# Optimization experiments

Hardware: AMD Instinct MI355X
Metric: run time of the kernel (lower is better)

## Reference

```python
import jax, jax.numpy as jnp
import numpy as np

N, E, F_IN, H, G, K = 50000, 800000, 64, 200, 256, 3


def setup_inputs() -> dict:
    key = jax.random.key(0)
    ks = jax.random.split(key, 12)
    x = jax.random.normal(ks[0], (N, F_IN), jnp.float32)
    edge_index = jax.random.randint(ks[1], (2, E), 0, N, dtype=jnp.int64)
    batch = jnp.sort(jax.random.randint(ks[2], (N,), 0, G, dtype=jnp.int64))
    lmax = 1.5 + jax.random.uniform(ks[3], (G,), jnp.float32)  # per-graph lambda_max

    def lin(k, i, o):
        return (jax.random.normal(k, (K, i, o), jnp.float32) / np.sqrt(i)).astype(jnp.float32)

    return dict(
        x=x, edge_index=edge_index, batch=batch, lmax=lmax,
        W1=lin(ks[4], F_IN, H), b1=jnp.zeros((H,), jnp.float32),
        W2=lin(ks[5], H, H),    b2=jnp.zeros((H,), jnp.float32),
        W3=lin(ks[6], H, H),    b3=jnp.zeros((H,), jnp.float32),
        W4=lin(ks[7], H, H),    b4=jnp.zeros((H,), jnp.float32),
        fc_w=(jax.random.normal(ks[8], (2 * H, 2), jnp.float32) / np.sqrt(2 * H)).astype(jnp.float32),
        fc_b=jnp.zeros((2,), jnp.float32),
    )


def reference(x, edge_index, batch, lmax, W1, b1, W2, b2, W3, b3, W4, b4, fc_w, fc_b):
    n = x.shape[0]
    g = lmax.shape[0]
    src, dst = edge_index[0], edge_index[1]

    # PyG ChebConv sym normalization: L_hat = 2/lambda_max * (I - D^-1/2 A D^-1/2) - I
    deg = jax.ops.segment_sum(jnp.ones(src.shape[0], x.dtype), src, num_segments=n)
    dis = jnp.where(deg > 0, jnp.maximum(deg, 1.0) ** -0.5, 0.0)  # deg^{-1/2}, inf -> 0
    scale = 2.0 / lmax                                            # [G]
    w = -dis[src] * dis[dst] * scale[batch[src]]                  # off-diagonal edge weights [E]
    diag = scale[batch] - 1.0                                     # diagonal of L_hat, [N]

    def prop(h):  # L_hat @ h via sparse scatter
        return jax.ops.segment_sum(w[:, None] * h[src], dst, num_segments=n) + diag[:, None] * h

    def cheb(h, W, b):  # K=3 Chebyshev recurrence
        Tx0 = h
        Tx1 = prop(h)
        Tx2 = 2.0 * prop(Tx1) - Tx0
        return Tx0 @ W[0] + Tx1 @ W[1] + Tx2 @ W[2] + b

    h = jax.nn.relu(cheb(x, W1, b1))
    h = jax.nn.relu(cheb(h, W2, b2))
    h = jax.nn.relu(cheb(h, W3, b3))
    h = jax.nn.relu(cheb(h, W4, b4))

    cnt = jax.ops.segment_sum(jnp.ones(n, h.dtype), batch, num_segments=g)
    pooled_mean = jax.ops.segment_sum(h, batch, num_segments=g) / jnp.maximum(cnt, 1.0)[:, None]
    pooled_max = jax.ops.segment_max(h, batch, num_segments=g)
    z = jnp.concatenate([pooled_mean, pooled_max], axis=1) @ fc_w + fc_b
    return jax.nn.log_softmax(z, axis=1)
```

## Files before the change

kernel.cpp:

```cpp
#include <hip/hip_runtime.h>
#include <math.h>

#define NN 50000
#define MP 50048
#define NE 800000
#define FIN 64
#define HD 200
#define NG 256
#define SCAN_B 256
#define KPAD 224
#define NT 13
#define HB 12544
#define PER_B 3125

typedef _Float16 h16;
typedef __attribute__((ext_vector_type(8))) _Float16 half8;
typedef __attribute__((ext_vector_type(4))) float float4v;
typedef unsigned long long u64;

__global__ __launch_bounds__(256) void k_hist(const int* __restrict__ idx,
                                              unsigned* __restrict__ partial, int E) {
    __shared__ unsigned h[HB];
    int tid = threadIdx.x;
    int e0 = blockIdx.x * PER_B;
    int v[13];
#pragma unroll
    for (int j = 0; j < 13; ++j) {
        int o = j * 256 + tid;
        v[j] = (o < PER_B) ? idx[e0 + o] : -1;
    }
#pragma unroll
    for (int pass = 0; pass < 2; ++pass) {
        for (int t = tid; t < HB; t += 256) h[t] = 0;
        __syncthreads();
        int lo = pass * (2 * HB);
#pragma unroll
        for (int j = 0; j < 13; ++j) {
            int vv = v[j] - lo;
            if (vv >= 0 && vv < 2 * HB)
                atomicAdd(&h[vv >> 1], (vv & 1) ? 0x10000u : 1u);
        }
        __syncthreads();
        unsigned* pb = partial + ((size_t)pass * 256 + blockIdx.x) * HB;
        for (int t = tid; t < HB; t += 256) pb[t] = h[t];
        __syncthreads();
    }
}

__global__ void k_hreduce(const unsigned* __restrict__ partial, int* __restrict__ cnt, int n) {
    int i = blockIdx.x * blockDim.x + threadIdx.x;
    if (i >= 2 * HB) return;
    int pass = i / HB, p = i - pass * HB;
    const unsigned* pb = partial + (size_t)pass * 256 * HB + p;
    unsigned s = 0;
    for (int b = 0; b < 256; ++b) s += pb[(size_t)b * HB];
    int n0 = pass * 2 * HB + 2 * p;
    if (n0 < n)     cnt[n0]     = (int)(s & 0xffffu);
    if (n0 + 1 < n) cnt[n0 + 1] = (int)(s >> 16);
}

__global__ void k_hscan(unsigned* __restrict__ partial, int* __restrict__ cnt, int n) {
    int i = blockIdx.x * blockDim.x + threadIdx.x;
    if (i >= 2 * HB) return;
    int pass = i / HB, p = i - pass * HB;
    unsigned* pb = partial + (size_t)pass * 256 * HB + p;
    unsigned run = 0;
    for (int b = 0; b < 256; ++b) {
        unsigned c = pb[(size_t)b * HB];
        pb[(size_t)b * HB] = run;
        run += c;
    }
    int n0 = pass * 2 * HB + 2 * p;
    if (n0 < n)     cnt[n0]     = (int)(run & 0xffffu);
    if (n0 + 1 < n) cnt[n0 + 1] = (int)(run >> 16);
}

__global__ void k_node_prep(const int* __restrict__ degi, const int* __restrict__ batch,
                            const float* __restrict__ lmax, float* __restrict__ dis,
                            float* __restrict__ qs, float* __restrict__ diag, int n) {
    int i = blockIdx.x * blockDim.x + threadIdx.x;
    if (i < n) {
        int d = degi[i];
        float di = (d > 0) ? (1.0f / sqrtf((float)d)) : 0.0f;
        float sc = 2.0f / lmax[batch[i]];
        dis[i] = di;
        qs[i] = -di * sc;
        diag[i] = sc - 1.0f;
    }
}

__global__ void k_scan1(const int* __restrict__ cnt, int* __restrict__ excl,
                        int* __restrict__ bsum, int n) {
    __shared__ int sh[SCAN_B];
    int tid = threadIdx.x;
    int i = blockIdx.x * SCAN_B + tid;
    int v = (i < n) ? cnt[i] : 0;
    sh[tid] = v;
    __syncthreads();
    for (int off = 1; off < SCAN_B; off <<= 1) {
        int t = (tid >= off) ? sh[tid - off] : 0;
        __syncthreads();
        sh[tid] += t;
        __syncthreads();
    }
    if (i < n) excl[i] = sh[tid] - v;
    if (tid == SCAN_B - 1) bsum[blockIdx.x] = sh[tid];
}

__global__ void k_scan2(int* __restrict__ bsum, int nb) {
    __shared__ int sh[SCAN_B];
    int tid = threadIdx.x;
    int v = (tid < nb) ? bsum[tid] : 0;
    sh[tid] = v;
    __syncthreads();
    for (int off = 1; off < SCAN_B; off <<= 1) {
        int t = (tid >= off) ? sh[tid - off] : 0;
        __syncthreads();
        sh[tid] += t;
        __syncthreads();
    }
    if (tid < nb) bsum[tid] = sh[tid] - v;
}

__global__ void k_scan3(int* __restrict__ excl, const int* __restrict__ bsum, int n) {
    int i = blockIdx.x * SCAN_B + threadIdx.x;
    if (i < n) excl[i] += bsum[blockIdx.x];
}

__global__ __launch_bounds__(256) void k_fillcsr2(
    const int* __restrict__ src, const int* __restrict__ dst,
    const float* __restrict__ qs, const float* __restrict__ dis,
    const int* __restrict__ rowst, const unsigned* __restrict__ hpart,
    u64* __restrict__ csr, int E) {
    __shared__ unsigned lrank[HB];
    int tid = threadIdx.x;
    int e0 = blockIdx.x * PER_B;
    int vs[13], vd[13];
#pragma unroll
    for (int j = 0; j < 13; ++j) {
        int o = j * 256 + tid;
        vs[j] = (o < PER_B) ? src[e0 + o] : -1;
        vd[j] = (o < PER_B) ? dst[e0 + o] : -1;
    }
#pragma unroll
    for (int pass = 0; pass < 2; ++pass) {
        for (int t = tid; t < HB; t += 256) lrank[t] = 0;
        __syncthreads();
        int lo = pass * (2 * HB);
        const unsigned* base = hpart + ((size_t)pass * 256 + blockIdx.x) * HB;
#pragma unroll
        for (int j = 0; j < 13; ++j) {
            int vv = vd[j] - lo;
            if (vv >= 0 && vv < 2 * HB) {
                unsigned old = atomicAdd(&lrank[vv >> 1], (vv & 1) ? 0x10000u : 1u);
                unsigned rank = (vv & 1) ? (old >> 16) : (old & 0xffffu);
                unsigned bs = base[vv >> 1];
                unsigned b = (vv & 1) ? (bs >> 16) : (bs & 0xffffu);
                int s = vs[j], d = vd[j];
                int pos = rowst[d] + (int)b + (int)rank;
                float w = qs[s] * dis[d];
                csr[pos] = (unsigned)s | ((u64)__float_as_uint(w) << 32);
            }
        }
        __syncthreads();
    }
}

__global__ void k_split(const float* __restrict__ x, h16* __restrict__ x16, int total) {
    int i = blockIdx.x * blockDim.x + threadIdx.x;
    if (i < total) x16[i] = (h16)x[i];
}

__global__ void k_wprep(const float* __restrict__ W, h16* __restrict__ out,
                        int fin, int ksteps, int total) {
    int idx = blockIdx.x * blockDim.x + threadIdx.x;
    if (idx >= total) return;
    int kk = idx & 31;
    int r = idx >> 5;
    int nn = r % 208;
    int r2 = r / 208;
    int ks = r2 % ksteps;
    int seg = r2 / ksteps;
    int k = ks * 32 + kk;
    out[idx] = (nn < HD && k < fin) ? (h16)W[((size_t)seg * fin + k) * HD + nn] : (h16)0.f;
}

__global__ void k_bounds(const int* __restrict__ batch, int* __restrict__ gstart, int n) {
    int g = blockIdx.x * blockDim.x + threadIdx.x;
    if (g > NG) return;
    if (g == NG) { gstart[NG] = n; return; }
    int lo = 0, hi = n;
    while (lo < hi) {
        int mid = (lo + hi) >> 1;
        if (batch[mid] < g) lo = mid + 1; else hi = mid;
    }
    gstart[g] = lo;
}

__global__ __launch_bounds__(256) void k_gather(
    const int* __restrict__ rowstart, const int* __restrict__ rowcnt,
    const u64* __restrict__ csr, const float* __restrict__ diag,
    const h16* __restrict__ hin16, const h16* __restrict__ h016,
    h16* __restrict__ hout16, int s16, int lsh, int n, int mode) {
    int per = 256 >> lsh;
    int i = blockIdx.x * per + (threadIdx.x >> lsh);
    if (i >= n) return;
    int lane = threadIdx.x & ((1 << lsh) - 1);
    int c0 = lane * 4;
    if (c0 >= s16) return;
    int start = rowstart[i], cnt = rowcnt[i];
    float a0 = 0.f, a1 = 0.f, a2 = 0.f, a3 = 0.f;
    union U { uint2 u; h16 h[4]; };
    const u64* cp = csr + start;
    int k = 0;
    for (; k + 7 < cnt; k += 8) {
        u64 e[8];
#pragma unroll
        for (int j = 0; j < 8; ++j) e[j] = cp[k + j];
        U p[8];
#pragma unroll
        for (int j = 0; j < 8; ++j)
            p[j].u = *(const uint2*)(hin16 + (size_t)(unsigned)(e[j] & 0xffffffffu) * s16 + c0);
#pragma unroll
        for (int j = 0; j < 8; ++j) {
            float w = __uint_as_float((unsigned)(e[j] >> 32));
            a0 += w * (float)p[j].h[0];
            a1 += w * (float)p[j].h[1];
            a2 += w * (float)p[j].h[2];
            a3 += w * (float)p[j].h[3];
        }
    }
    for (; k + 1 < cnt; k += 2) {
        u64 e0 = cp[k], e1 = cp[k + 1];
        U p0, p1;
        p0.u = *(const uint2*)(hin16 + (size_t)(unsigned)(e0 & 0xffffffffu) * s16 + c0);
        p1.u = *(const uint2*)(hin16 + (size_t)(unsigned)(e1 & 0xffffffffu) * s16 + c0);
        float w0 = __uint_as_float((unsigned)(e0 >> 32));
        float w1 = __uint_as_float((unsigned)(e1 >> 32));
        a0 += w0 * (float)p0.h[0] + w1 * (float)p1.h[0];
        a1 += w0 * (float)p0.h[1] + w1 * (float)p1.h[1];
        a2 += w0 * (float)p0.h[2] + w1 * (float)p1.h[2];
        a3 += w0 * (float)p0.h[3] + w1 * (float)p1.h[3];
    }
    if (k < cnt) {
        u64 e0 = cp[k];
        U p0;
        p0.u = *(const uint2*)(hin16 + (size_t)(unsigned)(e0 & 0xffffffffu) * s16 + c0);
        float w0 = __uint_as_float((unsigned)(e0 >> 32));
        a0 += w0 * (float)p0.h[0];
        a1 += w0 * (float)p0.h[1];
        a2 += w0 * (float)p0.h[2];
        a3 += w0 * (float)p0.h[3];
    }
    float dg = diag[i];
    U hs; hs.u = *(const uint2*)(hin16 + (size_t)i * s16 + c0);
    float v0 = a0 + dg * (float)hs.h[0];
    float v1 = a1 + dg * (float)hs.h[1];
    float v2 = a2 + dg * (float)hs.h[2];
    float v3 = a3 + dg * (float)hs.h[3];
    if (mode == 1) {
        U h0; h0.u = *(const uint2*)(h016 + (size_t)i * s16 + c0);
        v0 = 2.f * v0 - (float)h0.h[0];
        v1 = 2.f * v1 - (float)h0.h[1];
        v2 = 2.f * v2 - (float)h0.h[2];
        v3 = 2.f * v3 - (float)h0.h[3];
    }
    U o;
    o.h[0] = (h16)v0; o.h[1] = (h16)v1; o.h[2] = (h16)v2; o.h[3] = (h16)v3;
    *(uint2*)(hout16 + (size_t)i * s16 + c0) = o.u;
}

__global__ __launch_bounds__(256) void k_gemm16(
    const h16* __restrict__ A0, const h16* __restrict__ A1, const h16* __restrict__ A2,
    int strideA, int ksteps,
    const h16* __restrict__ Wt, const float* __restrict__ bias,
    h16* __restrict__ out16, int n) {
    int tid = threadIdx.x;
    int wave = tid >> 6, lane = tid & 63;
    int nq = lane & 15, quad = lane >> 4;
    int row0 = (blockIdx.x * 4 + wave) * 32;
    const h16* Aseg[3] = {A0, A1, A2};

    float4v acc[2][NT];
#pragma unroll
    for (int r = 0; r < 2; r++)
#pragma unroll
        for (int t = 0; t < NT; t++) acc[r][t] = (float4v)0.f;

    for (int seg = 0; seg < 3; ++seg) {
        const h16* Ab = Aseg[seg] + (size_t)(row0 + nq) * strideA + quad * 8;
        const h16* Bb = Wt + (size_t)seg * ksteps * 208 * 32 + (size_t)nq * 32 + quad * 8;
        for (int ks = 0; ks < ksteps; ++ks) {
            half8 af0 = *(const half8*)(Ab + ks * 32);
            half8 af1 = *(const half8*)(Ab + 16 * strideA + ks * 32);
            const h16* Bk = Bb + (size_t)ks * 208 * 32;
#pragma unroll
            for (int t = 0; t < NT; ++t) {
                half8 bf = *(const half8*)(Bk + t * 16 * 32);
                acc[0][t] = __builtin_amdgcn_mfma_f32_16x16x32_f16(af0, bf, acc[0][t], 0, 0, 0);
                acc[1][t] = __builtin_amdgcn_mfma_f32_16x16x32_f16(af1, bf, acc[1][t], 0, 0, 0);
            }
        }
    }
#pragma unroll
    for (int r = 0; r < 2; ++r) {
        int rowb = row0 + r * 16 + quad * 4;
#pragma unroll
        for (int t = 0; t < NT; ++t) {
            int col = t * 16 + nq;
            if (col >= HD) continue;
            float bj = bias[col];
#pragma unroll
            for (int g = 0; g < 4; ++g) {
                int row = rowb + g;
                if (row < n)
                    out16[(size_t)row * KPAD + col] = (h16)fmaxf(acc[r][t][g] + bj, 0.0f);
            }
        }
    }
}

__global__ __launch_bounds__(256) void k_pool_fc(
    const h16* __restrict__ Hf, const int* __restrict__ gstart,
    const float* __restrict__ fcw, const float* __restrict__ fcb,
    float* __restrict__ out) {
    __shared__ float red[8];
    int g = blockIdx.x;
    int j = threadIdx.x;
    int i0 = gstart[g], i1 = gstart[g + 1];
    float s0 = 0.f, s1 = 0.f, s2 = 0.f, s3 = 0.f, mx = 0.f;
    if (j < HD) {
        int i = i0;
        for (; i + 3 < i1; i += 4) {
            float v0 = (float)Hf[(size_t)i * KPAD + j];
            float v1 = (float)Hf[(size_t)(i + 1) * KPAD + j];
            float v2 = (float)Hf[(size_t)(i + 2) * KPAD + j];
            float v3 = (float)Hf[(size_t)(i + 3) * KPAD + j];
            s0 += v0; s1 += v1; s2 += v2; s3 += v3;
            mx = fmaxf(mx, fmaxf(fmaxf(v0, v1), fmaxf(v2, v3)));
        }
        for (; i < i1; ++i) {
            float v = (float)Hf[(size_t)i * KPAD + j];
            s0 += v; mx = fmaxf(mx, v);
        }
    }
    float cntf = (float)(i1 - i0);
    float mean = (s0 + s1 + s2 + s3) / fmaxf(cntf, 1.f);
    float p0 = 0.f, p1 = 0.f;
    if (j < HD) {
        p0 = mean * fcw[2 * j]     + mx * fcw[2 * (HD + j)];
        p1 = mean * fcw[2 * j + 1] + mx * fcw[2 * (HD + j) + 1];
    }
#pragma unroll
    for (int o = 32; o > 0; o >>= 1) {
        p0 += __shfl_down(p0, o);
        p1 += __shfl_down(p1, o);
    }
    int wave = j >> 6, lane = j & 63;
    if (lane == 0) { red[wave * 2] = p0; red[wave * 2 + 1] = p1; }
    __syncthreads();
    if (j == 0) {
        float z0 = red[0] + red[2] + red[4] + red[6] + fcb[0];
        float z1 = red[1] + red[3] + red[5] + red[7] + fcb[1];
        float m = fmaxf(z0, z1);
        float lse = m + logf(expf(z0 - m) + expf(z1 - m));
        out[g * 2 + 0] = z0 - lse;
        out[g * 2 + 1] = z1 - lse;
    }
}

extern "C" void kernel_launch(void* const* d_in, const int* in_sizes, int n_in,
                              void* d_out, int out_size, void* d_ws, size_t ws_size,
                              hipStream_t stream) {
    const float* x     = (const float*)d_in[0];
    const int*   edge  = (const int*)d_in[1];
    const int*   batch = (const int*)d_in[2];
    const float* lmax  = (const float*)d_in[3];
    const float* W1 = (const float*)d_in[4];  const float* b1 = (const float*)d_in[5];
    const float* W2 = (const float*)d_in[6];  const float* b2 = (const float*)d_in[7];
    const float* W3 = (const float*)d_in[8];  const float* b3 = (const float*)d_in[9];
    const float* W4 = (const float*)d_in[10]; const float* b4 = (const float*)d_in[11];
    const float* fcw = (const float*)d_in[12]; const float* fcb = (const float*)d_in[13];
    float* out = (float*)d_out;

    const int n = NN, E = NE;
    const int* src = edge;
    const int* dst = edge + E;

    float* ws = (float*)d_ws;
    size_t off = 0;
    auto alloc = [&](size_t nfloats) { float* p = ws + off; off += (nfloats + 3) & ~(size_t)3; return p; };
    int*   degi   = (int*)alloc(NN);
    float* dis    = alloc(NN);
    float* qs     = alloc(NN);
    float* diag   = alloc(NN);
    int*   cntd   = (int*)alloc(NN);
    int*   rowst  = (int*)alloc(NN);
    int*   bsum   = (int*)alloc(SCAN_B);
    u64*   csr    = (u64*)alloc((size_t)NE * 2);
    int*   gstart = (int*)alloc(NG + 1);
    unsigned* hpart = (unsigned*)alloc((size_t)2 * 256 * HB);
    h16*   x16    = (h16*)alloc((size_t)MP * FIN / 2);
    h16*   hi0    = (h16*)alloc((size_t)MP * KPAD / 2);
    h16*   hi1    = (h16*)alloc((size_t)MP * KPAD / 2);
    h16*   hi2    = (h16*)alloc((size_t)MP * KPAD / 2);
    const int WSZ0 = 3 * 2 * 208 * 32;
    const int WSZ  = 3 * 7 * 208 * 32;
    h16* wt0 = (h16*)alloc(WSZ0 / 2);
    h16* wt1 = (h16*)alloc(WSZ / 2);
    h16* wt2 = (h16*)alloc(WSZ / 2);
    h16* wt3 = (h16*)alloc(WSZ / 2);

    dim3 blk(256);
    int gE = (E + 255) / 256;
    int gN = (n + 255) / 256;
    int gScan = (n + SCAN_B - 1) / SCAN_B;
    int gGemm = MP / 128;
    int gHR = (2 * HB + 255) / 256;

    k_wprep<<<(WSZ0 + 255) / 256, blk, 0, stream>>>(W1, wt0, FIN, 2, WSZ0);
    k_wprep<<<(WSZ + 255) / 256, blk, 0, stream>>>(W2, wt1, HD, 7, WSZ);
    k_wprep<<<(WSZ + 255) / 256, blk, 0, stream>>>(W3, wt2, HD, 7, WSZ);
    k_wprep<<<(WSZ + 255) / 256, blk, 0, stream>>>(W4, wt3, HD, 7, WSZ);
    k_split<<<(NN * FIN + 255) / 256, blk, 0, stream>>>(x, x16, NN * FIN);
    k_bounds<<<2, blk, 0, stream>>>(batch, gstart, n);
    hipMemsetAsync(hi0, 0, (size_t)MP * KPAD * 2, stream);

    k_hist<<<256, blk, 0, stream>>>(src, hpart, E);
    k_hreduce<<<gHR, blk, 0, stream>>>(hpart, degi, n);
    k_hist<<<256, blk, 0, stream>>>(dst, hpart, E);
    k_hscan<<<gHR, blk, 0, stream>>>(hpart, cntd, n);
    k_node_prep<<<gN, blk, 0, stream>>>(degi, batch, lmax, dis, qs, diag, n);

    k_scan1<<<gScan, blk, 0, stream>>>(cntd, rowst, bsum, n);
    k_scan2<<<1, blk, 0, stream>>>(bsum, gScan);
    k_scan3<<<gScan, blk, 0, stream>>>(rowst, bsum, n);
    k_fillcsr2<<<256, blk, 0, stream>>>(src, dst, qs, dis, rowst, hpart, csr, E);

    const h16* wt[4] = {wt0, wt1, wt2, wt3};
    const float* bl[4] = {b1, b2, b3, b4};
    for (int l = 0; l < 4; l++) {
        int s16 = (l == 0) ? FIN : KPAD;
        int lsh = (l == 0) ? 4 : 6;
        int per = 256 >> lsh;
        int gGat = (n + per - 1) / per;
        int ksteps = (l == 0) ? 2 : 7;
        const h16* a0 = (l == 0) ? x16 : hi0;
        k_gather<<<gGat, blk, 0, stream>>>(rowst, cntd, csr, diag, a0, a0, hi1, s16, lsh, n, 0);
        k_gather<<<gGat, blk, 0, stream>>>(rowst, cntd, csr, diag, hi1, a0, hi2, s16, lsh, n, 1);
        k_gemm16<<<gGemm, blk, 0, stream>>>(a0, hi1, hi2, s16, ksteps, wt[l], bl[l],
                                            (l < 3) ? hi0 : hi1, n);
    }

    k_pool_fc<<<NG, blk, 0, stream>>>(hi1, gstart, fcw, fcb, out);
}
```

Before: 814.6 us.

## Fuse second Chebyshev propagation into GEMM kernel and merge setup launches

Adds k_gg, where each wave first runs the second sparse propagation (Tx2 = 2·L·Tx1 − Tx0) for its own 32 rows, then runs the MFMA GEMM over the three segments. This removes one gather launch per layer. Setup is also consolidated: the src/dst histograms run in one 512-block launch, the reduce and scan share a kernel, node prep and graph bounds are merged, the weight prep becomes a single launch, and the hi0 memset is dropped. The risk is that the fused gather runs with far fewer resident waves and 32 serial rows per wave, so latency hiding on the random loads may suffer. Padded columns of hi0 are also no longer zeroed.

```diff
diff --git a/kernel.cpp b/kernel.cpp
--- a/kernel.cpp
+++ b/kernel.cpp
@@ -18,11 +18,17 @@
 typedef __attribute__((ext_vector_type(4))) float float4v;
 typedef unsigned long long u64;
 
-__global__ __launch_bounds__(256) void k_hist(const int* __restrict__ idx,
-                                              unsigned* __restrict__ partial, int E) {
+__global__ __launch_bounds__(256) void k_hist(const int* __restrict__ src,
+                                              const int* __restrict__ dst,
+                                              unsigned* __restrict__ pSrc,
+                                              unsigned* __restrict__ pDst, int E) {
     __shared__ unsigned h[HB];
     int tid = threadIdx.x;
-    int e0 = blockIdx.x * PER_B;
+    int isDst = blockIdx.x >> 8;
+    int b = blockIdx.x & 255;
+    const int* idx = isDst ? dst : src;
+    unsigned* partial = isDst ? pDst : pSrc;
+    int e0 = b * PER_B;
     int v[13];
 #pragma unroll
     for (int j = 0; j < 13; ++j) {
@@ -41,51 +47,64 @@
                 atomicAdd(&h[vv >> 1], (vv & 1) ? 0x10000u : 1u);
         }
         __syncthreads();
-        unsigned* pb = partial + ((size_t)pass * 256 + blockIdx.x) * HB;
+        unsigned* pb = partial + ((size_t)pass * 256 + b) * HB;
         for (int t = tid; t < HB; t += 256) pb[t] = h[t];
         __syncthreads();
     }
 }
 
-__global__ void k_hreduce(const unsigned* __restrict__ partial, int* __restrict__ cnt, int n) {
+__global__ void k_hredscan(const unsigned* __restrict__ pSrc, unsigned* __restrict__ pDst,
+                           int* __restrict__ degi, int* __restrict__ cntd, int n) {
     int i = blockIdx.x * blockDim.x + threadIdx.x;
-    if (i >= 2 * HB) return;
-    int pass = i / HB, p = i - pass * HB;
-    const unsigned* pb = partial + (size_t)pass * 256 * HB + p;
-    unsigned s = 0;
-    for (int b = 0; b < 256; ++b) s += pb[(size_t)b * HB];
-    int n0 = pass * 2 * HB + 2 * p;
-    if (n0 < n)     cnt[n0]     = (int)(s & 0xffffu);
-    if (n0 + 1 < n) cnt[n0 + 1] = (int)(s >> 16);
-}
-
-__global__ void k_hscan(unsigned* __restrict__ partial, int* __restrict__ cnt, int n) {
-    int i = blockIdx.x * blockDim.x + threadIdx.x;
-    if (i >= 2 * HB) return;
-    int pass = i / HB, p = i - pass * HB;
-    unsigned* pb = partial + (size_t)pass * 256 * HB + p;
-    unsigned run = 0;
-    for (int b = 0; b < 256; ++b) {
-        unsigned c = pb[(size_t)b * HB];
-        pb[(size_t)b * HB] = run;
-        run += c;
-    }
-    int n0 = pass * 2 * HB + 2 * p;
-    if (n0 < n)     cnt[n0]     = (int)(run & 0xffffu);
-    if (n0 + 1 < n) cnt[n0 + 1] = (int)(run >> 16);
-}
-
-__global__ void k_node_prep(const int* __restrict__ degi, const int* __restrict__ batch,
-                            const float* __restrict__ lmax, float* __restrict__ dis,
-                            float* __restrict__ qs, float* __restrict__ diag, int n) {
-    int i = blockIdx.x * blockDim.x + threadIdx.x;
-    if (i < n) {
-        int d = degi[i];
-        float di = (d > 0) ? (1.0f / sqrtf((float)d)) : 0.0f;
-        float sc = 2.0f / lmax[batch[i]];
-        dis[i] = di;
-        qs[i] = -di * sc;
-        diag[i] = sc - 1.0f;
+    if (i < 2 * HB) {
+        int pass = i / HB, p = i - pass * HB;
+        const unsigned* pb = pSrc + (size_t)pass * 256 * HB + p;
+        unsigned s = 0;
+        for (int b = 0; b < 256; ++b) s += pb[(size_t)b * HB];
+        int n0 = pass * 2 * HB + 2 * p;
+        if (n0 < n)     degi[n0]     = (int)(s & 0xffffu);
+        if (n0 + 1 < n) degi[n0 + 1] = (int)(s >> 16);
+    } else if (i < 4 * HB) {
+        int j = i - 2 * HB;
+        int pass = j / HB, p = j - pass * HB;
+        unsigned* pb = pDst + (size_t)pass * 256 * HB + p;
+        unsigned run = 0;
+        for (int b = 0; b < 256; ++b) {
+            unsigned c = pb[(size_t)b * HB];
+            pb[(size_t)b * HB] = run;
+            run += c;
+        }
+        int n0 = pass * 2 * HB + 2 * p;
+        if (n0 < n)     cntd[n0]     = (int)(run & 0xffffu);
+        if (n0 + 1 < n) cntd[n0 + 1] = (int)(run >> 16);
+    }
+}
+
+__global__ void k_prep(const int* __restrict__ degi, const int* __restrict__ batch,
+                       const float* __restrict__ lmax, float* __restrict__ dis,
+                       float* __restrict__ qs, float* __restrict__ diag,
+                       int* __restrict__ gstart, int n, int gN) {
+    int b = blockIdx.x;
+    if (b < gN) {
+        int i = b * 256 + threadIdx.x;
+        if (i < n) {
+            int d = degi[i];
+            float di = (d > 0) ? (1.0f / sqrtf((float)d)) : 0.0f;
+            float sc = 2.0f / lmax[batch[i]];
+            dis[i] = di;
+            qs[i] = -di * sc;
+            diag[i] = sc - 1.0f;
+        }
+    } else {
+        int g = (b - gN) * 256 + threadIdx.x;
+        if (g > NG) return;
+        if (g == NG) { gstart[NG] = n; return; }
+        int lo = 0, hi = n;
+        while (lo < hi) {
+            int mid = (lo + hi) >> 1;
+            if (batch[mid] < g) lo = mid + 1; else hi = mid;
+        }
+        gstart[g] = lo;
     }
 }
 
@@ -155,9 +174,9 @@
                 unsigned old = atomicAdd(&lrank[vv >> 1], (vv & 1) ? 0x10000u : 1u);
                 unsigned rank = (vv & 1) ? (old >> 16) : (old & 0xffffu);
                 unsigned bs = base[vv >> 1];
-                unsigned b = (vv & 1) ? (bs >> 16) : (bs & 0xffffu);
+                unsigned bb = (vv & 1) ? (bs >> 16) : (bs & 0xffffu);
                 int s = vs[j], d = vd[j];
-                int pos = rowst[d] + (int)b + (int)rank;
+                int pos = rowst[d] + (int)bb + (int)rank;
                 float w = qs[s] * dis[d];
                 csr[pos] = (unsigned)s | ((u64)__float_as_uint(w) << 32);
             }
@@ -171,37 +190,36 @@
     if (i < total) x16[i] = (h16)x[i];
 }
 
-__global__ void k_wprep(const float* __restrict__ W, h16* __restrict__ out,
-                        int fin, int ksteps, int total) {
+__global__ void k_wprep(const float* __restrict__ W1, const float* __restrict__ W2,
+                        const float* __restrict__ W3, const float* __restrict__ W4,
+                        h16* __restrict__ wt0, h16* __restrict__ wt1,
+                        h16* __restrict__ wt2, h16* __restrict__ wt3) {
+    const int T0 = 3 * 2 * 208 * 32, T = 3 * 7 * 208 * 32;
     int idx = blockIdx.x * blockDim.x + threadIdx.x;
-    if (idx >= total) return;
-    int kk = idx & 31;
-    int r = idx >> 5;
-    int nn = r % 208;
-    int r2 = r / 208;
-    int ks = r2 % ksteps;
-    int seg = r2 / ksteps;
+    const float* W; h16* o; int fin, ksteps, li;
+    if (idx < T0) { W = W1; o = wt0; fin = FIN; ksteps = 2; li = idx; }
+    else {
+        int r = idx - T0; int l = r / T;
+        if (l > 2) return;
+        li = r - l * T; fin = HD; ksteps = 7;
+        W = (l == 0) ? W2 : ((l == 1) ? W3 : W4);
+        o = (l == 0) ? wt1 : ((l == 1) ? wt2 : wt3);
+    }
+    int kk = li & 31;
+    int r2 = li >> 5;
+    int nn = r2 % 208;
+    int r3 = r2 / 208;
+    int ks = r3 % ksteps;
+    int seg = r3 / ksteps;
     int k = ks * 32 + kk;
-    out[idx] = (nn < HD && k < fin) ? (h16)W[((size_t)seg * fin + k) * HD + nn] : (h16)0.f;
-}
-
-__global__ void k_bounds(const int* __restrict__ batch, int* __restrict__ gstart, int n) {
-    int g = blockIdx.x * blockDim.x + threadIdx.x;
-    if (g > NG) return;
-    if (g == NG) { gstart[NG] = n; return; }
-    int lo = 0, hi = n;
-    while (lo < hi) {
-        int mid = (lo + hi) >> 1;
-        if (batch[mid] < g) lo = mid + 1; else hi = mid;
-    }
-    gstart[g] = lo;
+    o[li] = (nn < HD && k < fin) ? (h16)W[((size_t)seg * fin + k) * HD + nn] : (h16)0.f;
 }
 
 __global__ __launch_bounds__(256) void k_gather(
     const int* __restrict__ rowstart, const int* __restrict__ rowcnt,
     const u64* __restrict__ csr, const float* __restrict__ diag,
-    const h16* __restrict__ hin16, const h16* __restrict__ h016,
-    h16* __restrict__ hout16, int s16, int lsh, int n, int mode) {
+    const h16* __restrict__ hin16, h16* __restrict__ hout16,
+    int s16, int lsh, int n) {
     int per = 256 >> lsh;
     int i = blockIdx.x * per + (threadIdx.x >> lsh);
     if (i >= n) return;
@@ -209,7 +227,7 @@
     int c0 = lane * 4;
     if (c0 >= s16) return;
     int start = rowstart[i], cnt = rowcnt[i];
-    float a0 = 0.f, a1 = 0.f, a2 = 0.f, a3 = 0.f;
+    float g0 = 0.f, g1 = 0.f, g2 = 0.f, g3 = 0.f;
     union U { uint2 u; h16 h[4]; };
     const u64* cp = csr + start;
     int k = 0;
@@ -224,63 +242,98 @@
 #pragma unroll
         for (int j = 0; j < 8; ++j) {
             float w = __uint_as_float((unsigned)(e[j] >> 32));
-            a0 += w * (float)p[j].h[0];
-            a1 += w * (float)p[j].h[1];
-            a2 += w * (float)p[j].h[2];
-            a3 += w * (float)p[j].h[3];
-        }
-    }
-    for (; k + 1 < cnt; k += 2) {
-        u64 e0 = cp[k], e1 = cp[k + 1];
-        U p0, p1;
-        p0.u = *(const uint2*)(hin16 + (size_t)(unsigned)(e0 & 0xffffffffu) * s16 + c0);
-        p1.u = *(const uint2*)(hin16 + (size_t)(unsigned)(e1 & 0xffffffffu) * s16 + c0);
-        float w0 = __uint_as_float((unsigned)(e0 >> 32));
-        float w1 = __uint_as_float((unsigned)(e1 >> 32));
-        a0 += w0 * (float)p0.h[0] + w1 * (float)p1.h[0];
-        a1 += w0 * (float)p0.h[1] + w1 * (float)p1.h[1];
-        a2 += w0 * (float)p0.h[2] + w1 * (float)p1.h[2];
-        a3 += w0 * (float)p0.h[3] + w1 * (float)p1.h[3];
-    }
-    if (k < cnt) {
+            g0 += w * (float)p[j].h[0];
+            g1 += w * (float)p[j].h[1];
+            g2 += w * (float)p[j].h[2];
+            g3 += w * (float)p[j].h[3];
+        }
+    }
+    for (; k < cnt; ++k) {
         u64 e0 = cp[k];
         U p0;
         p0.u = *(const uint2*)(hin16 + (size_t)(unsigned)(e0 & 0xffffffffu) * s16 + c0);
-        float w0 = __uint_as_float((unsigned)(e0 >> 32));
-        a0 += w0 * (float)p0.h[0];
-        a1 += w0 * (float)p0.h[1];
-        a2 += w0 * (float)p0.h[2];
-        a3 += w0 * (float)p0.h[3];
+        float w = __uint_as_float((unsigned)(e0 >> 32));
+        g0 += w * (float)p0.h[0];
+        g1 += w * (float)p0.h[1];
+        g2 += w * (float)p0.h[2];
+        g3 += w * (float)p0.h[3];
     }
     float dg = diag[i];
     U hs; hs.u = *(const uint2*)(hin16 + (size_t)i * s16 + c0);
-    float v0 = a0 + dg * (float)hs.h[0];
-    float v1 = a1 + dg * (float)hs.h[1];
-    float v2 = a2 + dg * (float)hs.h[2];
-    float v3 = a3 + dg * (float)hs.h[3];
-    if (mode == 1) {
-        U h0; h0.u = *(const uint2*)(h016 + (size_t)i * s16 + c0);
-        v0 = 2.f * v0 - (float)h0.h[0];
-        v1 = 2.f * v1 - (float)h0.h[1];
-        v2 = 2.f * v2 - (float)h0.h[2];
-        v3 = 2.f * v3 - (float)h0.h[3];
-    }
     U o;
-    o.h[0] = (h16)v0; o.h[1] = (h16)v1; o.h[2] = (h16)v2; o.h[3] = (h16)v3;
+    o.h[0] = (h16)(g0 + dg * (float)hs.h[0]);
+    o.h[1] = (h16)(g1 + dg * (float)hs.h[1]);
+    o.h[2] = (h16)(g2 + dg * (float)hs.h[2]);
+    o.h[3] = (h16)(g3 + dg * (float)hs.h[3]);
     *(uint2*)(hout16 + (size_t)i * s16 + c0) = o.u;
 }
 
-__global__ __launch_bounds__(256) void k_gemm16(
-    const h16* __restrict__ A0, const h16* __restrict__ A1, const h16* __restrict__ A2,
-    int strideA, int ksteps,
+__global__ __launch_bounds__(256) void k_gg(
+    const int* __restrict__ rowstart, const int* __restrict__ rowcnt,
+    const u64* __restrict__ csr, const float* __restrict__ diag,
+    const h16* hin, const h16* a0p, h16* tx2,
+    int s16, int ksteps,
     const h16* __restrict__ Wt, const float* __restrict__ bias,
-    h16* __restrict__ out16, int n) {
+    h16* out16, int n) {
     int tid = threadIdx.x;
     int wave = tid >> 6, lane = tid & 63;
+    int row0 = (blockIdx.x * 4 + wave) * 32;
+    union U { uint2 u; h16 h[4]; };
+
+    int nsub   = (s16 == FIN) ? 4 : 1;
+    int rounds = 32 / nsub;
+    int sl     = (s16 == FIN) ? (lane >> 4) : 0;
+    int cl     = (s16 == FIN) ? ((lane & 15) * 4) : (lane * 4);
+    if (cl < s16) {
+        for (int r = 0; r < rounds; ++r) {
+            int i = row0 + r * nsub + sl;
+            if (i >= n) continue;
+            int start = rowstart[i], cnt = rowcnt[i];
+            const u64* cp = csr + start;
+            float g0 = 0.f, g1 = 0.f, g2 = 0.f, g3 = 0.f;
+            int k = 0;
+            for (; k + 7 < cnt; k += 8) {
+                u64 e[8];
+#pragma unroll
+                for (int j = 0; j < 8; ++j) e[j] = cp[k + j];
+                U p[8];
+#pragma unroll
+                for (int j = 0; j < 8; ++j)
+                    p[j].u = *(const uint2*)(hin + (size_t)(unsigned)(e[j] & 0xffffffffu) * s16 + cl);
+#pragma unroll
+                for (int j = 0; j < 8; ++j) {
+                    float w = __uint_as_float((unsigned)(e[j] >> 32));
+                    g0 += w * (float)p[j].h[0];
+                    g1 += w * (float)p[j].h[1];
+                    g2 += w * (float)p[j].h[2];
+                    g3 += w * (float)p[j].h[3];
+                }
+            }
+            for (; k < cnt; ++k) {
+                u64 e0 = cp[k];
+                U p0;
+                p0.u = *(const uint2*)(hin + (size_t)(unsigned)(e0 & 0xffffffffu) * s16 + cl);
+                float w = __uint_as_float((unsigned)(e0 >> 32));
+                g0 += w * (float)p0.h[0];
+                g1 += w * (float)p0.h[1];
+                g2 += w * (float)p0.h[2];
+                g3 += w * (float)p0.h[3];
+            }
+            float dg = diag[i];
+            U hs; hs.u = *(const uint2*)(hin + (size_t)i * s16 + cl);
+            U h0; h0.u = *(const uint2*)(a0p + (size_t)i * s16 + cl);
+            U o;
+            o.h[0] = (h16)(2.f * (g0 + dg * (float)hs.h[0]) - (float)h0.h[0]);
+            o.h[1] = (h16)(2.f * (g1 + dg * (float)hs.h[1]) - (float)h0.h[1]);
+            o.h[2] = (h16)(2.f * (g2 + dg * (float)hs.h[2]) - (float)h0.h[2]);
+            o.h[3] = (h16)(2.f * (g3 + dg * (float)hs.h[3]) - (float)h0.h[3]);
+            *(uint2*)(tx2 + (size_t)i * s16 + cl) = o.u;
+        }
+    }
+    __threadfence_block();
+
     int nq = lane & 15, quad = lane >> 4;
-    int row0 = (blockIdx.x * 4 + wave) * 32;
-    const h16* Aseg[3] = {A0, A1, A2};
-
+    const h16* Aseg[3] = {a0p, hin, tx2};
     float4v acc[2][NT];
 #pragma unroll
     for (int r = 0; r < 2; r++)
@@ -288,11 +341,11 @@
         for (int t = 0; t < NT; t++) acc[r][t] = (float4v)0.f;
 
     for (int seg = 0; seg < 3; ++seg) {
-        const h16* Ab = Aseg[seg] + (size_t)(row0 + nq) * strideA + quad * 8;
+        const h16* Ab = Aseg[seg] + (size_t)(row0 + nq) * s16 + quad * 8;
         const h16* Bb = Wt + (size_t)seg * ksteps * 208 * 32 + (size_t)nq * 32 + quad * 8;
         for (int ks = 0; ks < ksteps; ++ks) {
             half8 af0 = *(const half8*)(Ab + ks * 32);
-            half8 af1 = *(const half8*)(Ab + 16 * strideA + ks * 32);
+            half8 af1 = *(const half8*)(Ab + 16 * s16 + ks * 32);
             const h16* Bk = Bb + (size_t)ks * 208 * 32;
 #pragma unroll
             for (int t = 0; t < NT; ++t) {
@@ -399,11 +452,13 @@
     int*   bsum   = (int*)alloc(SCAN_B);
     u64*   csr    = (u64*)alloc((size_t)NE * 2);
     int*   gstart = (int*)alloc(NG + 1);
-    unsigned* hpart = (unsigned*)alloc((size_t)2 * 256 * HB);
+    unsigned* pSrc = (unsigned*)alloc((size_t)2 * 256 * HB);
+    unsigned* pDst = (unsigned*)alloc((size_t)2 * 256 * HB);
     h16*   x16    = (h16*)alloc((size_t)MP * FIN / 2);
     h16*   hi0    = (h16*)alloc((size_t)MP * KPAD / 2);
     h16*   hi1    = (h16*)alloc((size_t)MP * KPAD / 2);
     h16*   hi2    = (h16*)alloc((size_t)MP * KPAD / 2);
+    h16*   hi3    = (h16*)alloc((size_t)MP * KPAD / 2);
     const int WSZ0 = 3 * 2 * 208 * 32;
     const int WSZ  = 3 * 7 * 208 * 32;
     h16* wt0 = (h16*)alloc(WSZ0 / 2);
@@ -412,30 +467,20 @@
     h16* wt3 = (h16*)alloc(WSZ / 2);
 
     dim3 blk(256);
-    int gE = (E + 255) / 256;
     int gN = (n + 255) / 256;
     int gScan = (n + SCAN_B - 1) / SCAN_B;
     int gGemm = MP / 128;
-    int gHR = (2 * HB + 255) / 256;
-
-    k_wprep<<<(WSZ0 + 255) / 256, blk, 0, stream>>>(W1, wt0, FIN, 2, WSZ0);
-    k_wprep<<<(WSZ + 255) / 256, blk, 0, stream>>>(W2, wt1, HD, 7, WSZ);
-    k_wprep<<<(WSZ + 255) / 256, blk, 0, stream>>>(W3, wt2, HD, 7, WSZ);
-    k_wprep<<<(WSZ + 255) / 256, blk, 0, stream>>>(W4, wt3, HD, 7, WSZ);
+    int gWp = (WSZ0 + 3 * WSZ + 255) / 256;
+
+    k_wprep<<<gWp, blk, 0, stream>>>(W1, W2, W3, W4, wt0, wt1, wt2, wt3);
     k_split<<<(NN * FIN + 255) / 256, blk, 0, stream>>>(x, x16, NN * FIN);
-    k_bounds<<<2, blk, 0, stream>>>(batch, gstart, n);
-    hipMemsetAsync(hi0, 0, (size_t)MP * KPAD * 2, stream);
-
-    k_hist<<<256, blk, 0, stream>>>(src, hpart, E);
-    k_hreduce<<<gHR, blk, 0, stream>>>(hpart, degi, n);
-    k_hist<<<256, blk, 0, stream>>>(dst, hpart, E);
-    k_hscan<<<gHR, blk, 0, stream>>>(hpart, cntd, n);
-    k_node_prep<<<gN, blk, 0, stream>>>(degi, batch, lmax, dis, qs, diag, n);
-
+    k_hist<<<512, blk, 0, stream>>>(src, dst, pSrc, pDst, E);
+    k_hredscan<<<(4 * HB + 255) / 256, blk, 0, stream>>>(pSrc, pDst, degi, cntd, n);
+    k_prep<<<gN + 2, blk, 0, stream>>>(degi, batch, lmax, dis, qs, diag, gstart, n, gN);
     k_scan1<<<gScan, blk, 0, stream>>>(cntd, rowst, bsum, n);
     k_scan2<<<1, blk, 0, stream>>>(bsum, gScan);
     k_scan3<<<gScan, blk, 0, stream>>>(rowst, bsum, n);
-    k_fillcsr2<<<256, blk, 0, stream>>>(src, dst, qs, dis, rowst, hpart, csr, E);
+    k_fillcsr2<<<256, blk, 0, stream>>>(src, dst, qs, dis, rowst, pDst, csr, E);
 
     const h16* wt[4] = {wt0, wt1, wt2, wt3};
     const float* bl[4] = {b1, b2, b3, b4};
@@ -446,11 +491,11 @@
         int gGat = (n + per - 1) / per;
         int ksteps = (l == 0) ? 2 : 7;
         const h16* a0 = (l == 0) ? x16 : hi0;
-        k_gather<<<gGat, blk, 0, stream>>>(rowst, cntd, csr, diag, a0, a0, hi1, s16, lsh, n, 0);
-        k_gather<<<gGat, blk, 0, stream>>>(rowst, cntd, csr, diag, hi1, a0, hi2, s16, lsh, n, 1);
-        k_gemm16<<<gGemm, blk, 0, stream>>>(a0, hi1, hi2, s16, ksteps, wt[l], bl[l],
-                                            (l < 3) ? hi0 : hi1, n);
-    }
-
-    k_pool_fc<<<NG, blk, 0, stream>>>(hi1, gstart, fcw, fcb, out);
-}
+        k_gather<<<gGat, blk, 0, stream>>>(rowst, cntd, csr, diag, a0, hi1, s16, lsh, n);
+        k_gg<<<gGemm, blk, 0, stream>>>(rowst, cntd, csr, diag, hi1, a0, hi2,
+                                        s16, ksteps, wt[l], bl[l],
+                                        (l < 3) ? hi0 : hi3, n);
+    }
+
+    k_pool_fc<<<NG, blk, 0, stream>>>(hi3, gstart, fcw, fcb, out);
+}
```

After: 1.023 ms. +25.6%, slower.
